# Optimization experiments

Hardware: AMD Instinct MI355X
Metric: run time of the kernel (lower is better)

## Reference

```python
import jax, jax.numpy as jnp
import numpy as np

IN_F = 4096
OUT_F = 4096
BLOCK_SIZE = 64
BLOCK_NUM = 64
N_FACTOR = 2  # number of butterfly factor matrices (boft_n_butterfly_factor after internal -1, +1)


def block_butterfly_perm(n, b, r, nf):
    # faithful port of BOFTLayer.block_butterfly_perm (static numpy computation)
    if nf == 0:
        return np.arange(n)
    block_size = n // b
    indices = np.arange(n)
    step = block_size / r
    evens = np.arange(0, step, 2)
    odds = np.arange(1, step, 2)
    sorted_seq = np.concatenate([evens, odds]).astype(np.int64)
    sorted_order = np.empty(block_size, dtype=np.int64)
    for i, pos in enumerate(sorted_seq):
        sorted_order[i * r:(i + 1) * r] = np.arange(pos * r, pos * r + r)
    perm = indices.copy()
    for i in range(0, n, block_size):
        perm[i:i + block_size] = indices[i:i + block_size][sorted_order]
    return perm


def _perms():
    return [block_butterfly_perm(IN_F, BLOCK_NUM // (2 ** i), BLOCK_SIZE // 2, N_FACTOR - 1)
            for i in range(N_FACTOR)]


def cayley_batch(R):
    # Q = (I - skew) @ (I + skew)^{-1}, solved as Q (I+skew) = (I-skew)
    skew = 0.5 * (R - jnp.swapaxes(R, -1, -2))
    I = jnp.eye(R.shape[-1], dtype=R.dtype)
    Qt = jnp.linalg.solve(jnp.swapaxes(I + skew, -1, -2), jnp.swapaxes(I - skew, -1, -2))
    return jnp.swapaxes(Qt, -1, -2)


def block_diag_batch(blocks):
    # [D,H,H] -> [D*H, D*H] block-diagonal
    D, H, _ = blocks.shape
    out = jnp.zeros((D * H, D * H), blocks.dtype)
    r = jnp.arange(D)[:, None, None] * H + jnp.arange(H)[None, :, None]
    c = jnp.arange(D)[:, None, None] * H + jnp.arange(H)[None, None, :]
    return out.at[r, c].set(blocks)


def setup_inputs() -> dict:
    key = jax.random.key(0)
    k1, k2, k3, k4 = jax.random.split(key, 4)
    x = jax.random.normal(k1, (2, 2048, IN_F), dtype=jnp.float32)
    weight = jax.random.normal(k2, (OUT_F, IN_F), dtype=jnp.float32) * 0.02
    bias = jax.random.normal(k3, (OUT_F,), dtype=jnp.float32) * 0.02
    boft_R = jax.random.normal(k4, (N_FACTOR, BLOCK_NUM, BLOCK_SIZE, BLOCK_SIZE), dtype=jnp.float32) * 0.1
    boft_s = jnp.ones((OUT_F, 1), dtype=jnp.float32)
    return {"x": x, "weight": weight, "bias": bias, "boft_R": boft_R, "boft_s": boft_s}


def reference(x, weight, bias, boft_R, boft_s):
    N, D, H, _ = boft_R.shape
    Q = cayley_batch(boft_R.reshape(N * D, H, H)).reshape(N, D, H, H)
    perms = _perms()
    rot = jnp.eye(IN_F, dtype=x.dtype)
    for i in range(N):
        B = block_diag_batch(Q[i])                         # [in, in]
        p = perms[i]
        Bp = B[p[:, None], p[None, :]]                     # P @ B @ P^T
        rot = Bp @ rot                                     # compose butterfly factors
    # rotated weight: (rot @ W^T)^T = W @ rot^T, then per-output scaling
    scaled_w = (weight @ rot.T) * boft_s                   # [out, in]
    return x @ scaled_w.T + bias
```

## Files before the change

### kernel.cpp

```cpp
#include <hip/hip_runtime.h>

typedef unsigned short u16;
typedef unsigned int   u32;
typedef __attribute__((ext_vector_type(4))) float f32x4;
typedef __attribute__((ext_vector_type(8))) short bf16x8;
typedef __attribute__((ext_vector_type(4))) unsigned short u16x4;
typedef __attribute__((ext_vector_type(8))) unsigned short u16x8;

__device__ __forceinline__ u16 f2bf(float f) {
  union { float f; u32 u; } v; v.f = f;
  u32 r = v.u + 0x7FFFu + ((v.u >> 16) & 1u);
  return (u16)(r >> 16);
}

__device__ __forceinline__ float bcast(float v, int l) {
  return __uint_as_float(__builtin_amdgcn_readlane(__float_as_uint(v), l));
}

__global__ __launch_bounds__(256, 1) void cayley_kernel(
    const float* __restrict__ R, float* __restrict__ Q) {
  const int b  = blockIdx.x;
  const int t  = threadIdx.x;
  const int j  = t & 63;
  const int iw = t >> 6;
  __shared__ float Rl[64][65];
  __shared__ float prow[2][2][64];
  const float* Rb = R + (size_t)b * 4096;
  for (int idx = t; idx < 4096; idx += 256)
    Rl[idx >> 6][idx & 63] = Rb[idx];
  __syncthreads();
  float Ac[16], Bc[16];
  #pragma unroll
  for (int i2 = 0; i2 < 16; ++i2) {
    const int i = iw*16 + i2;
    float s = 0.5f * (Rl[i][j] - Rl[j][i]);
    Ac[i2] = (i == j) ? (1.0f + s) : s;
    Bc[i2] = (i == j) ? 1.0f : 0.0f;
  }
  __syncthreads();
  #pragma unroll
  for (int kb = 0; kb < 4; ++kb) {
    #pragma unroll
    for (int kp = 0; kp < 16; ++kp) {
      const int k = kb*16 + kp;
      if (iw == kb) {
        float pinv = 1.0f / bcast(Ac[kp], k);
        float ar = Ac[kp] * pinv;
        float br = Bc[kp] * pinv;
        Ac[kp] = ar; Bc[kp] = br;
        prow[k & 1][0][j] = ar;
        prow[k & 1][1][j] = br;
      }
      __syncthreads();
      const float ar = prow[k & 1][0][j];
      const float br = prow[k & 1][1][j];
      #pragma unroll
      for (int i2 = 0; i2 < 16; ++i2) {
        float f = bcast(Ac[i2], k);
        if (iw == kb && i2 == kp) f = 0.0f;
        Ac[i2] -= f * ar;
        Bc[i2] -= f * br;
      }
    }
  }
  float* Qb = Q + (size_t)b * 4096;
  #pragma unroll
  for (int i2 = 0; i2 < 16; ++i2) {
    const int i = iw*16 + i2;
    Qb[i*64 + j] = 2.0f * Bc[i2] - ((i == j) ? 1.0f : 0.0f);
  }
}

__global__ __launch_bounds__(256) void rotbuild_kernel(
    const float* __restrict__ Q, u16* __restrict__ rotb) {
  const int s = blockIdx.x;
  const int t = threadIdx.x;
  __shared__ float Q1l[2][64][65];
  __shared__ f32x4 Q0l[2][64][16];
  const float* Q0g = Q + (size_t)(2*s) * 4096;
  const float* Q1g = Q + (size_t)(64 + 2*s) * 4096;
  for (int i = t; i < 2*4096; i += 256) {
    int e = i >> 12, r = (i >> 6) & 63, c = i & 63;
    Q1l[e][r][c] = Q1g[i];
    ((float*)&Q0l[e][r][0])[c] = Q0g[i];
  }
  __syncthreads();
  const int a_l = t & 127;
  const int dh  = t >> 7;
  const int g   = a_l >> 5;
  const int pa  = a_l + ((g == 1) ? 32 : (g == 2) ? -32 : 0);
  const int e = pa >> 6, pa64 = pa & 63;
  float q1v[32];
  #pragma unroll
  for (int jj = 0; jj < 32; ++jj) q1v[jj] = Q1l[e][pa64][dh*32 + jj];
  f32x4 acc4[16] = {};
  #pragma unroll
  for (int jj = 0; jj < 32; ++jj) {
    #pragma unroll
    for (int c4 = 0; c4 < 16; ++c4)
      acc4[c4] += q1v[jj] * Q0l[dh][e*32 + jj][c4];
  }
  u16* dst = rotb + (size_t)s*16384 + (size_t)a_l*128 + dh*64;
  #pragma unroll
  for (int c4 = 0; c4 < 16; ++c4) {
    u16x4 o;
    o.x = f2bf(acc4[c4].x); o.y = f2bf(acc4[c4].y);
    o.z = f2bf(acc4[c4].z); o.w = f2bf(acc4[c4].w);
    *(u16x4*)&dst[c4*4] = o;
  }
}

__global__ __launch_bounds__(256) void wtrans_kernel(
    const float* __restrict__ W, const u16* __restrict__ rotb,
    const float* __restrict__ sscale, u16* __restrict__ SW) {
  const int rt = blockIdx.x;
  const int s  = blockIdx.y;
  const int t  = threadIdx.x;
  __shared__ u16 Asw[128*128];
  __shared__ u16 Bsw[128*128];
  #pragma unroll
  for (int p = 0; p < 16; ++p) {
    const int g = p*256 + t;
    const int row = g >> 5, gc = g & 31;
    float4 v = *(const float4*)(W + (size_t)(rt*128 + row)*4096 + s*128 + gc*4);
    u16x4 o;
    o.x = f2bf(v.x); o.y = f2bf(v.y); o.z = f2bf(v.z); o.w = f2bf(v.w);
    const int chunk = (gc >> 1) ^ (row & 7);
    *(u16x4*)&Asw[row*128 + chunk*8 + (gc & 1)*4] = o;
  }
  const u16* rsrc = rotb + (size_t)s*16384;
  #pragma unroll
  for (int p = 0; p < 8; ++p) {
    const int g = p*256 + t;
    const int row = g >> 4, ch = g & 15;
    u16x8 v = *(const u16x8*)(rsrc + row*128 + ch*8);
    *(u16x8*)&Bsw[row*128 + ((ch ^ (row & 7))*8)] = v;
  }
  __syncthreads();
  const int w = t >> 6, l = t & 63;
  const int fr = l & 15, fq = l >> 4;
  const int wm = (w >> 1)*64, wn = (w & 1)*64;
  f32x4 acc[4][4] = {};
  #pragma unroll
  for (int ks = 0; ks < 4; ++ks) {
    bf16x8 af[4], bfr[4];
    #pragma unroll
    for (int m = 0; m < 4; ++m)
      af[m] = *(const bf16x8*)&Asw[(wm + m*16 + fr)*128 + (((ks*4 + fq) ^ (fr & 7))*8)];
    #pragma unroll
    for (int n = 0; n < 4; ++n)
      bfr[n] = *(const bf16x8*)&Bsw[(wn + n*16 + fr)*128 + (((ks*4 + fq) ^ (fr & 7))*8)];
    #pragma unroll
    for (int m = 0; m < 4; ++m)
      #pragma unroll
      for (int n = 0; n < 4; ++n)
        acc[m][n] = __builtin_amdgcn_mfma_f32_16x16x32_bf16(
            af[m], bfr[n], acc[m][n], 0, 0, 0);
  }
  #pragma unroll
  for (int m = 0; m < 4; ++m) {
    #pragma unroll
    for (int r = 0; r < 4; ++r) {
      const int row = rt*128 + wm + m*16 + fq*4 + r;
      const float sc = sscale[row];
      #pragma unroll
      for (int n = 0; n < 4; ++n) {
        const int col = s*128 + wn + n*16 + fr;
        SW[(size_t)row*4096 + col] = f2bf(acc[m][n][r] * sc);
      }
    }
  }
}

__global__ __launch_bounds__(256) void cvt_kernel(
    const float* __restrict__ x, u16* __restrict__ xb) {
  #pragma unroll
  for (int rep = 0; rep < 4; ++rep) {
    const size_t i = (size_t)(rep*2048 + blockIdx.x) * 256 + threadIdx.x;
    const float4* p = (const float4*)x + i*2;
    float4 a = p[0], b = p[1];
    u16x8 o;
    o[0] = f2bf(a.x); o[1] = f2bf(a.y); o[2] = f2bf(a.z); o[3] = f2bf(a.w);
    o[4] = f2bf(b.x); o[5] = f2bf(b.y); o[6] = f2bf(b.z); o[7] = f2bf(b.w);
    *(u16x8*)(xb + i*8) = o;
  }
}

#define GLDS16(g, l)                                                   \
  __builtin_amdgcn_global_load_lds(                                    \
      (const __attribute__((address_space(1))) void*)(g),              \
      (__attribute__((address_space(3))) void*)(l), 16, 0, 0)

__device__ __forceinline__ void bar() {
  asm volatile("" ::: "memory");
  __builtin_amdgcn_s_barrier();
  asm volatile("" ::: "memory");
}

__global__ __launch_bounds__(512, 2) void gemm_kernel(
    const u16* __restrict__ A, const u16* __restrict__ B,
    const float* __restrict__ bias, float* __restrict__ C) {
  constexpr int K = 4096, N = 4096, NT = 64;
  __shared__ u16 As[2*256*64];
  __shared__ u16 Bs[2*256*64];
  const int t = threadIdx.x;
  const int w = t >> 6, l = t & 63;
  const int wr = w >> 2, wc = w & 3;
  const int fr = l & 15, fq = l >> 4;

  const int wg  = blockIdx.x;
  const int swz = (wg & 7) * 32 + (wg >> 3);
  const int m0  = (swz & 15) * 256, n0 = (swz >> 4) * 256;

  const int grow = w*8 + (l >> 3);
  const int gcol = ((l & 7) ^ ((l >> 3) & 7)) * 8;
  const u16* aS = A + (size_t)(m0 + grow) * K + gcol;
  const u16* bS = B + (size_t)(n0 + grow) * K + gcol;
  const int wLds = w * 512;

  const int colbase = (fq ^ (fr & 7)) * 8;
  const u16* aRd = As + (wr*128 + fr)*64;
  const u16* bRd = Bs + (wc*64  + fr)*64;

  auto stgA = [&](int buf, int half, int o, int kt_) {
    GLDS16(aS + (size_t)(half*128 + o*64) * K + (size_t)kt_*64,
           As + buf*16384 + half*8192 + o*4096 + wLds);
  };
  auto stgB = [&](int buf, int half, int o, int kt_) {
    GLDS16(bS + (size_t)(half*128 + o*64) * K + (size_t)kt_*64,
           Bs + buf*16384 + half*8192 + o*4096 + wLds);
  };

  f32x4 acc[8][4] = {};
  bf16x8 aF[4][2], bF[4][2];

  auto rdA = [&](int buf, int mh) {
    const u16* aC = aRd + buf*16384;
    #pragma unroll
    for (int m = 0; m < 4; ++m) {
      aF[m][0] = *(const bf16x8*)(aC + (mh*4 + m)*1024 + colbase);
      aF[m][1] = *(const bf16x8*)(aC + (mh*4 + m)*1024 + (colbase ^ 32));
    }
  };
  auto rdB = [&](int buf, int nh) {
    const u16* bC = bRd + buf*16384;
    #pragma unroll
    for (int n = 0; n < 2; ++n) {
      bF[nh*2 + n][0] = *(const bf16x8*)(bC + (nh*2 + n)*1024 + colbase);
      bF[nh*2 + n][1] = *(const bf16x8*)(bC + (nh*2 + n)*1024 + (colbase ^ 32));
    }
  };
  auto mma = [&](int mh, int nh) {
    __builtin_amdgcn_s_setprio(1);
    #pragma unroll
    for (int ks = 0; ks < 2; ++ks)
      #pragma unroll
      for (int m = 0; m < 4; ++m)
        #pragma unroll
        for (int n = 0; n < 2; ++n)
          acc[mh*4 + m][nh*2 + n] = __builtin_amdgcn_mfma_f32_16x16x32_bf16(
              aF[m][ks], bF[nh*2 + n][ks], acc[mh*4 + m][nh*2 + n], 0, 0, 0);
    __builtin_amdgcn_s_setprio(0);
  };

  stgB(0,0,0,0); stgB(0,0,1,0); stgB(0,1,0,0); stgB(0,1,1,0);
  stgA(0,0,0,0); stgA(0,0,1,0); stgA(0,1,0,0); stgA(0,1,1,0);
  stgB(1,0,0,1); stgB(1,0,1,1); stgB(1,1,0,1); stgB(1,1,1,1);
  stgA(1,0,0,1); stgA(1,0,1,1); stgA(1,1,0,1); stgA(1,1,1,1);
  asm volatile("s_waitcnt vmcnt(8)" ::: "memory");
  bar();
  rdA(0, 0); rdB(0, 0);

  for (int kt = 0; kt < NT; ++kt) {
    const int cur = kt & 1;
    mma(0, 0);
    rdB(cur, 1);
    mma(0, 1);
    rdA(cur, 1);
    bar();
    if (kt + 2 < NT) { stgB(cur,0,0,kt+2); stgB(cur,0,1,kt+2); }
    mma(1, 1);
    if (kt + 2 < NT) { stgB(cur,1,0,kt+2); stgB(cur,1,1,kt+2); }
    if (kt < NT - 2) {
      asm volatile("s_waitcnt vmcnt(4)" ::: "memory");
    } else if (kt == NT - 2) {
      asm volatile("s_waitcnt vmcnt(0)" ::: "memory");
    }
    bar();
    if (kt + 2 < NT) { stgA(cur,0,0,kt+2); stgA(cur,0,1,kt+2); }
    mma(1, 0);
    if (kt + 2 < NT) { stgA(cur,1,0,kt+2); stgA(cur,1,1,kt+2); }
    if (kt + 1 < NT) { rdA(cur ^ 1, 0); rdB(cur ^ 1, 0); }
  }

  #pragma unroll
  for (int nf = 0; nf < 4; ++nf) {
    const int col = n0 + wc*64 + nf*16 + fr;
    const float bv = bias[col];
    #pragma unroll
    for (int mf = 0; mf < 8; ++mf) {
      const int rowb = m0 + wr*128 + mf*16 + fq*4;
      #pragma unroll
      for (int r = 0; r < 4; ++r)
        C[(size_t)(rowb + r)*N + col] = acc[mf][nf][r] + bv;
    }
  }
}

extern "C" void kernel_launch(void* const* d_in, const int* in_sizes, int n_in,
                              void* d_out, int out_size, void* d_ws, size_t ws_size,
                              hipStream_t stream) {
  const float* x      = (const float*)d_in[0];
  const float* W      = (const float*)d_in[1];
  const float* bias   = (const float*)d_in[2];
  const float* boft_R = (const float*)d_in[3];
  const float* boft_s = (const float*)d_in[4];
  float* out = (float*)d_out;

  char* ws = (char*)d_ws;
  float* Q    = (float*)ws;
  u16*   rotb = (u16*)  (ws + ((size_t)2  << 20));
  u16*   xb   = (u16*)  (ws + ((size_t)4  << 20));
  u16*   swb  = (u16*)  (ws + ((size_t)36 << 20));

  cayley_kernel  <<<128, 256, 0, stream>>>(boft_R, Q);
  rotbuild_kernel<<<32, 256, 0, stream>>>(Q, rotb);
  wtrans_kernel  <<<dim3(32, 32), 256, 0, stream>>>(W, rotb, boft_s, swb);
  cvt_kernel     <<<2048, 256, 0, stream>>>(x, xb);
  gemm_kernel    <<<256, 512, 0, stream>>>(xb, swb, bias, out);
}
```

Before: 192.6 us.

## Switch GEMM inner loop from 16x16x32 to 32x32x16 bf16 MFMA tiles

Replaces the 16x16x32 MFMA tiling with 32x32x16 MFMA instructions, restructuring the LDS fragment reads per k-slice with a new XOR swizzle offset, the register fragment layout and the epilogue row mapping. Larger MFMA tiles cut the number of LDS fragment loads per FLOP and the instruction issue count. In exchange the pipeline now double-buffers fragments by k-slice, and the accumulator layout changes, which could affect register pressure and LDS bank conflicts.

```diff
diff --git a/kernel.cpp b/kernel.cpp
--- a/kernel.cpp
+++ b/kernel.cpp
@@ -3,6 +3,7 @@
 typedef unsigned short u16;
 typedef unsigned int   u32;
 typedef __attribute__((ext_vector_type(4))) float f32x4;
+typedef __attribute__((ext_vector_type(16))) float f32x16;
 typedef __attribute__((ext_vector_type(8))) short bf16x8;
 typedef __attribute__((ext_vector_type(4))) unsigned short u16x4;
 typedef __attribute__((ext_vector_type(8))) unsigned short u16x8;
@@ -206,7 +207,7 @@
   const int t = threadIdx.x;
   const int w = t >> 6, l = t & 63;
   const int wr = w >> 2, wc = w & 3;
-  const int fr = l & 15, fq = l >> 4;
+  const int l31 = l & 31, fq5 = l >> 5, r7 = l & 7;
 
   const int wg  = blockIdx.x;
   const int swz = (wg & 7) * 32 + (wg >> 3);
@@ -218,9 +219,8 @@
   const u16* bS = B + (size_t)(n0 + grow) * K + gcol;
   const int wLds = w * 512;
 
-  const int colbase = (fq ^ (fr & 7)) * 8;
-  const u16* aRd = As + (wr*128 + fr)*64;
-  const u16* bRd = Bs + (wc*64  + fr)*64;
+  const u16* aRd = As + (wr*128 + l31)*64;
+  const u16* bRd = Bs + (wc*64  + l31)*64;
 
   auto stgA = [&](int buf, int half, int o, int kt_) {
     GLDS16(aS + (size_t)(half*128 + o*64) * K + (size_t)kt_*64,
@@ -231,35 +231,31 @@
            Bs + buf*16384 + half*8192 + o*4096 + wLds);
   };
 
-  f32x4 acc[8][4] = {};
-  bf16x8 aF[4][2], bF[4][2];
-
-  auto rdA = [&](int buf, int mh) {
+  f32x16 acc[4][2] = {};
+  bf16x8 aF[4][2], bF[2][2];
+
+  auto rdA = [&](int buf, int ks, int slot) {
     const u16* aC = aRd + buf*16384;
-    #pragma unroll
-    for (int m = 0; m < 4; ++m) {
-      aF[m][0] = *(const bf16x8*)(aC + (mh*4 + m)*1024 + colbase);
-      aF[m][1] = *(const bf16x8*)(aC + (mh*4 + m)*1024 + (colbase ^ 32));
-    }
-  };
-  auto rdB = [&](int buf, int nh) {
+    const int off = ((ks*2 + fq5) ^ r7) * 8;
+    #pragma unroll
+    for (int mt = 0; mt < 4; ++mt)
+      aF[mt][slot] = *(const bf16x8*)(aC + mt*2048 + off);
+  };
+  auto rdB = [&](int buf, int ks, int slot) {
     const u16* bC = bRd + buf*16384;
-    #pragma unroll
-    for (int n = 0; n < 2; ++n) {
-      bF[nh*2 + n][0] = *(const bf16x8*)(bC + (nh*2 + n)*1024 + colbase);
-      bF[nh*2 + n][1] = *(const bf16x8*)(bC + (nh*2 + n)*1024 + (colbase ^ 32));
-    }
-  };
-  auto mma = [&](int mh, int nh) {
+    const int off = ((ks*2 + fq5) ^ r7) * 8;
+    #pragma unroll
+    for (int nt = 0; nt < 2; ++nt)
+      bF[nt][slot] = *(const bf16x8*)(bC + nt*2048 + off);
+  };
+  auto mmaKS = [&](int slot) {
     __builtin_amdgcn_s_setprio(1);
     #pragma unroll
-    for (int ks = 0; ks < 2; ++ks)
-      #pragma unroll
-      for (int m = 0; m < 4; ++m)
-        #pragma unroll
-        for (int n = 0; n < 2; ++n)
-          acc[mh*4 + m][nh*2 + n] = __builtin_amdgcn_mfma_f32_16x16x32_bf16(
-              aF[m][ks], bF[nh*2 + n][ks], acc[mh*4 + m][nh*2 + n], 0, 0, 0);
+    for (int mt = 0; mt < 4; ++mt)
+      #pragma unroll
+      for (int nt = 0; nt < 2; ++nt)
+        acc[mt][nt] = __builtin_amdgcn_mfma_f32_32x32x16_bf16(
+            aF[mt][slot], bF[nt][slot], acc[mt][nt], 0, 0, 0);
     __builtin_amdgcn_s_setprio(0);
   };
 
@@ -269,17 +265,18 @@
   stgA(1,0,0,1); stgA(1,0,1,1); stgA(1,1,0,1); stgA(1,1,1,1);
   asm volatile("s_waitcnt vmcnt(8)" ::: "memory");
   bar();
-  rdA(0, 0); rdB(0, 0);
+  rdA(0, 0, 0); rdB(0, 0, 0);
+  rdA(0, 1, 1); rdB(0, 1, 1);
 
   for (int kt = 0; kt < NT; ++kt) {
     const int cur = kt & 1;
-    mma(0, 0);
-    rdB(cur, 1);
-    mma(0, 1);
-    rdA(cur, 1);
+    mmaKS(0);
+    rdA(cur, 2, 0); rdB(cur, 2, 0);
+    mmaKS(1);
+    rdA(cur, 3, 1); rdB(cur, 3, 1);
     bar();
     if (kt + 2 < NT) { stgB(cur,0,0,kt+2); stgB(cur,0,1,kt+2); }
-    mma(1, 1);
+    mmaKS(0);
     if (kt + 2 < NT) { stgB(cur,1,0,kt+2); stgB(cur,1,1,kt+2); }
     if (kt < NT - 2) {
       asm volatile("s_waitcnt vmcnt(4)" ::: "memory");
@@ -288,21 +285,26 @@
     }
     bar();
     if (kt + 2 < NT) { stgA(cur,0,0,kt+2); stgA(cur,0,1,kt+2); }
-    mma(1, 0);
+    mmaKS(1);
     if (kt + 2 < NT) { stgA(cur,1,0,kt+2); stgA(cur,1,1,kt+2); }
-    if (kt + 1 < NT) { rdA(cur ^ 1, 0); rdB(cur ^ 1, 0); }
-  }
-
-  #pragma unroll
-  for (int nf = 0; nf < 4; ++nf) {
-    const int col = n0 + wc*64 + nf*16 + fr;
+    if (kt + 1 < NT) {
+      rdA(cur ^ 1, 0, 0); rdB(cur ^ 1, 0, 0);
+      rdA(cur ^ 1, 1, 1); rdB(cur ^ 1, 1, 1);
+    }
+  }
+
+  #pragma unroll
+  for (int nt = 0; nt < 2; ++nt) {
+    const int col = n0 + wc*64 + nt*32 + l31;
     const float bv = bias[col];
     #pragma unroll
-    for (int mf = 0; mf < 8; ++mf) {
-      const int rowb = m0 + wr*128 + mf*16 + fq*4;
-      #pragma unroll
-      for (int r = 0; r < 4; ++r)
-        C[(size_t)(rowb + r)*N + col] = acc[mf][nf][r] + bv;
+    for (int mt = 0; mt < 4; ++mt) {
+      const int rowb = m0 + wr*128 + mt*32 + 4*fq5;
+      #pragma unroll
+      for (int r = 0; r < 16; ++r) {
+        const int row = rowb + (r & 3) + 8*(r >> 2);
+        C[(size_t)row*N + col] = acc[mt][nt][r] + bv;
+      }
     }
   }
 }
```

Measured after the change: 205.4 us. +6.6%, slower.
